# Performance work log

Measured on AMD Instinct MI355X. Metric: run time of the kernel, lower is better.

## Reference

```python
import jax, jax.numpy as jnp
import numpy as np

NEG_SLOPE = 0.2
H = 2  # num_heads (hardcoded in the torch module)


def _gat_conv(x, W, al, ar, b, src, dst, n_nodes):
    """DGL GATConv: x [N,F] -> [N,H,D]."""
    D = al.shape[1]
    h = (x @ W).reshape(n_nodes, H, D)               # [N,H,D]
    el = jnp.einsum('nhd,hd->nh', h, al)              # [N,H]
    er = jnp.einsum('nhd,hd->nh', h, ar)              # [N,H]
    e = el[src] + er[dst]                             # [E,H]
    e = jnp.where(e >= 0, e, NEG_SLOPE * e)           # LeakyReLU
    # edge softmax over incoming edges of each dst (every node has a self loop)
    m = jax.ops.segment_max(e, dst, num_segments=n_nodes)      # [N,H]
    ex = jnp.exp(e - m[dst])                                    # [E,H]
    s = jax.ops.segment_sum(ex, dst, num_segments=n_nodes)     # [N,H]
    alpha = ex / s[dst]                                         # [E,H]
    msg = alpha[:, :, None] * h[src]                             # [E,H,D]
    out = jax.ops.segment_sum(msg, dst, num_segments=n_nodes)   # [N,H,D]
    return out + b.reshape(1, H, D)


def setup_inputs() -> dict:
    key = jax.random.key(0)
    ks = jax.random.split(key, 10)
    N, E, F_IN, HID, OUT = 100000, 1600000, 128, 64, 64
    sc = 0.05
    return {
        'x':   jax.random.normal(ks[0], (N, F_IN), jnp.float32),
        'src': jax.random.randint(ks[1], (E,), 0, N, jnp.int32),
        'dst': jax.random.randint(ks[2], (E,), 0, N, jnp.int32),
        'W1':  jax.random.normal(ks[3], (F_IN, H * HID), jnp.float32) * sc,
        'al1': jax.random.normal(ks[4], (H, HID), jnp.float32) * sc,
        'ar1': jax.random.normal(ks[5], (H, HID), jnp.float32) * sc,
        'b1':  jnp.zeros((H * HID,), jnp.float32),
        'W2':  jax.random.normal(ks[6], (H * HID, H * OUT), jnp.float32) * sc,
        'al2': jax.random.normal(ks[7], (H, OUT), jnp.float32) * sc,
        'ar2': jax.random.normal(ks[8], (H, OUT), jnp.float32) * sc,
        'b2':  jnp.zeros((H * OUT,), jnp.float32),
    }


def reference(x, src, dst, W1, al1, ar1, b1, W2, al2, ar2, b2):
    N = x.shape[0]
    # dgl.add_self_loop
    loop = jnp.arange(N, dtype=src.dtype)
    s = jnp.concatenate([src, loop])
    d = jnp.concatenate([dst, loop])
    h = _gat_conv(x, W1, al1, ar1, b1, s, d, N)       # [N,H,HID]
    h = jax.nn.relu(h).reshape(N, -1)                  # flatten heads
    out = _gat_conv(h, W2, al2, ar2, b2, s, d, N)      # [N,H,OUT]
    return out.reshape(N, -1)
```

## Files before the change

### kernel.cpp

```cpp
#include <hip/hip_runtime.h>
#include <hip/hip_fp16.h>


#define NEG_SLOPE 0.2f
#define BSHIFT 8
#define ETILE 4096

typedef _Float16 half8_t __attribute__((ext_vector_type(8)));
typedef float f32x4_t __attribute__((ext_vector_type(4)));
typedef unsigned long long u64;


__global__ __launch_bounds__(256) void k_bscan(const int* __restrict__ bcnt, int nbuck,
                                               int* __restrict__ bbase,
                                               int* __restrict__ bcursor,
                                               int* __restrict__ rowStart, int N, int E) {
    __shared__ int sa[512], sb[512];
    int t = threadIdx.x;
    sa[t] = (t < nbuck) ? bcnt[t] : 0;
    sa[t + 256] = (t + 256 < nbuck) ? bcnt[t + 256] : 0;
    __syncthreads();
    int* a = sa;
    int* b = sb;
    for (int off = 1; off < 512; off <<= 1) {
        b[t] = a[t] + ((t >= off) ? a[t - off] : 0);
        int i = t + 256;
        b[i] = a[i] + ((i >= off) ? a[i - off] : 0);
        __syncthreads();
        int* tmp = a; a = b; b = tmp;
    }
    #pragma unroll
    for (int k = 0; k < 2; k++) {
        int i = t + k * 256;
        if (i <= nbuck) {
            int e_ = (i == 0) ? 0 : a[i - 1];
            bbase[i] = e_;
            if (i < nbuck) bcursor[i] = e_;
        }
    }
    if (t == 0) rowStart[N] = E;
}

__global__ __launch_bounds__(256) void k_bucket(const int* __restrict__ src,
                                                const int* __restrict__ dst, int E,
                                                int nbuck, int* __restrict__ bcursor,
                                                int* __restrict__ ebuf) {
    __shared__ int cnt[512];
    __shared__ int base[512];
    int t = threadIdx.x;
    for (int b = t; b < nbuck; b += 256) cnt[b] = 0;
    __syncthreads();
    int e0 = blockIdx.x * ETILE;
    int dv[ETILE / 256], sv[ETILE / 256];
    #pragma unroll
    for (int j = 0; j < ETILE / 256; j++) {
        int e = e0 + j * 256 + t;
        dv[j] = -1;
        if (e < E) {
            dv[j] = dst[e];
            sv[j] = src[e];
            atomicAdd(&cnt[dv[j] >> BSHIFT], 1);
        }
    }
    __syncthreads();
    for (int b = t; b < nbuck; b += 256) {
        int c = cnt[b];
        base[b] = (c > 0) ? atomicAdd(&bcursor[b], c) : 0;
    }
    __syncthreads();
    for (int b = t; b < nbuck; b += 256) cnt[b] = 0;
    __syncthreads();
    #pragma unroll
    for (int j = 0; j < ETILE / 256; j++) {
        if (dv[j] >= 0) {
            int bk = dv[j] >> BSHIFT;
            int r = atomicAdd(&cnt[bk], 1);
            ebuf[base[bk] + r] = sv[j] | ((dv[j] & ((1 << BSHIFT) - 1)) << 17);
        }
    }
}

__global__ __launch_bounds__(256) void k_build(const int* __restrict__ ebuf,
                                               const int* __restrict__ bbase,
                                               int* __restrict__ rowStart,
                                               int* __restrict__ csr, int N) {
    __shared__ int dcnt[256];
    __shared__ int sa[256], sb[256];
    __shared__ int cur[256];
    int b = blockIdx.x;
    int t = threadIdx.x;
    int lo = bbase[b], hi = bbase[b + 1];
    int n0 = b << BSHIFT;
    dcnt[t] = 0;
    __syncthreads();
    for (int p = lo + t; p < hi; p += 256)
        atomicAdd(&dcnt[((unsigned)ebuf[p]) >> 17], 1);
    __syncthreads();
    sa[t] = dcnt[t];
    __syncthreads();
    int* a = sa;
    int* bq = sb;
    for (int off = 1; off < 256; off <<= 1) {
        bq[t] = a[t] + ((t >= off) ? a[t - off] : 0);
        __syncthreads();
        int* tmp = a; a = bq; bq = tmp;
    }
    int excl = (t == 0) ? 0 : a[t - 1];
    int pos0 = lo + excl;
    if (n0 + t < N) rowStart[n0 + t] = pos0;
    cur[t] = pos0;
    __syncthreads();
    for (int p = lo + t; p < hi; p += 256) {
        int v = ebuf[p];
        int pos = atomicAdd(&cur[((unsigned)v) >> 17], 1);
        csr[pos] = v & 0x1FFFF;
    }
}


__global__ __launch_bounds__(256) void k_prep(const float* __restrict__ W1,
                                              const float* __restrict__ W2,
                                              __half* __restrict__ wh1,
                                              __half* __restrict__ wh2,
                                              int* __restrict__ bcnt, int nbuck) {
    int b = blockIdx.x;
    if (b >= 16) {
        for (int i = threadIdx.x; i < nbuck; i += 256) bcnt[i] = 0;
        return;
    }
    const float* W = (b < 8) ? W1 : W2;
    __half* Wh = (b < 8) ? wh1 : wh2;
    int q = (b & 7) * 256 + threadIdx.x;
    int r = q >> 4;
    int c = q & 15;
    int cl = c ^ (r & 7);
    float f[8];
    #pragma unroll
    for (int j = 0; j < 8; j++) f[j] = W[(size_t)(cl * 8 + j) * 128 + r];
    __half2 h0 = __floats2half2_rn(f[0], f[1]);
    __half2 h1 = __floats2half2_rn(f[2], f[3]);
    __half2 h2 = __floats2half2_rn(f[4], f[5]);
    __half2 h3 = __floats2half2_rn(f[6], f[7]);
    uint4 pk;
    pk.x = *(unsigned*)&h0;
    pk.y = *(unsigned*)&h1;
    pk.z = *(unsigned*)&h2;
    pk.w = *(unsigned*)&h3;
    *(uint4*)((char*)Wh + (size_t)q * 16) = pk;
}


__device__ __forceinline__ void g2l16(const void* g, void* l) {
    __builtin_amdgcn_global_load_lds((const __attribute__((address_space(1))) void*)g,
                                     (__attribute__((address_space(3))) void*)l, 16, 0, 0);
}

template <bool FP16IN, bool COUNT>
__global__ __launch_bounds__(256, 3) void k_gemm_fused(const void* __restrict__ Ain,
                                                       const __half* __restrict__ WhT,
                                                       __half* __restrict__ hb,
                                                       const float* __restrict__ al,
                                                       const float* __restrict__ ar,
                                                       float* __restrict__ el,
                                                       float* __restrict__ er, int M,
                                                       const int* __restrict__ dstE, int E,
                                                       int nbuck, int* __restrict__ bcnt,
                                                       int gemmBlocks) {
    __shared__ __half xs[64 * 128];
    __shared__ __half ws[128 * 128];
    int t = threadIdx.x;

    if (COUNT && (int)blockIdx.x >= gemmBlocks) {
        int* cnt = (int*)xs;
        for (int b = t; b < nbuck; b += 256) cnt[b] = 0;
        __syncthreads();
        int e0 = ((int)blockIdx.x - gemmBlocks) * ETILE;
        #pragma unroll
        for (int j = 0; j < ETILE / 256; j++) {
            int e = e0 + j * 256 + t;
            if (e < E) atomicAdd(&cnt[dstE[e] >> BSHIFT], 1);
        }
        __syncthreads();
        for (int b = t; b < nbuck; b += 256) {
            int c = cnt[b];
            if (c > 0) atomicAdd(&bcnt[b], c);
        }
        return;
    }

    int row0 = blockIdx.x * 64;
    for (int j = 0; j < 8; j++) {
        int c16 = t + j * 256;
        g2l16((const char*)WhT + (size_t)c16 * 16, (char*)ws + (size_t)c16 * 16);
    }
    if (FP16IN) {
        const char* Ah = (const char*)Ain;
        for (int j = 0; j < 4; j++) {
            int c16 = t + j * 256;
            g2l16(Ah + (size_t)row0 * 256 + (size_t)c16 * 16, (char*)xs + (size_t)c16 * 16);
        }
    } else {
        const float* A = (const float*)Ain;
        for (int j = 0; j < 8; j++) {
            int f4 = t + j * 256;
            int r = f4 >> 5;
            int gr = row0 + r;
            if (gr >= M) gr = M - 1;
            float4 v = ((const float4*)(A + (size_t)gr * 128))[f4 & 31];
            __half2 h0 = __floats2half2_rn(v.x, v.y);
            __half2 h1 = __floats2half2_rn(v.z, v.w);
            uint2 pk;
            pk.x = *(unsigned*)&h0;
            pk.y = *(unsigned*)&h1;
            int h8 = f4 & 31;
            int c = h8 >> 1, hh = h8 & 1;
            int addr8 = r * 32 + (c ^ (r & 7)) * 2 + hh;
            *(uint2*)((char*)xs + (size_t)addr8 * 8) = pk;
        }
    }
    __syncthreads();

    int wid = t >> 6, lane = t & 63;
    int l15 = lane & 15;
    int g = lane >> 4;
    int mrow = wid * 16 + l15;

    half8_t xf[4];
    #pragma unroll
    for (int ks = 0; ks < 4; ks++) {
        int c = ks * 4 + g;
        xf[ks] = *(const half8_t*)((const char*)xs + mrow * 256 + (size_t)(c ^ (mrow & 7)) * 16);
    }

    f32x4_t acc[8];
    #pragma unroll
    for (int i = 0; i < 8; i++) acc[i] = (f32x4_t){0.f, 0.f, 0.f, 0.f};

    #pragma unroll
    for (int nt = 0; nt < 8; nt++) {
        int nrow = nt * 16 + l15;
        #pragma unroll
        for (int ks = 0; ks < 4; ks++) {
            int c = ks * 4 + g;
            half8_t wf = *(const half8_t*)((const char*)ws + nrow * 256 + (size_t)(c ^ (nrow & 7)) * 16);
            acc[nt] = __builtin_amdgcn_mfma_f32_16x16x32_f16(wf, xf[ks], acc[nt], 0, 0, 0);
        }
    }

    int m = row0 + wid * 16 + l15;
    bool valid = m < M;
    float plh0 = 0.f, prh0 = 0.f, plh1 = 0.f, prh1 = 0.f;
    #pragma unroll
    for (int nt = 0; nt < 8; nt++) {
        int col0 = nt * 16 + g * 4;
        if (valid) {
            __half2 p0 = __floats2half2_rn(acc[nt][0], acc[nt][1]);
            __half2 p1 = __floats2half2_rn(acc[nt][2], acc[nt][3]);
            uint2 pk;
            pk.x = *(unsigned*)&p0;
            pk.y = *(unsigned*)&p1;
            *(uint2*)(hb + (size_t)m * 128 + col0) = pk;
        }
        float4 alv = *(const float4*)(al + col0);
        float4 arv = *(const float4*)(ar + col0);
        float pl = acc[nt][0] * alv.x + acc[nt][1] * alv.y + acc[nt][2] * alv.z + acc[nt][3] * alv.w;
        float pr = acc[nt][0] * arv.x + acc[nt][1] * arv.y + acc[nt][2] * arv.z + acc[nt][3] * arv.w;
        if (nt < 4) { plh0 += pl; prh0 += pr; }
        else       { plh1 += pl; prh1 += pr; }
    }
    plh0 += __shfl_xor(plh0, 16); plh0 += __shfl_xor(plh0, 32);
    plh1 += __shfl_xor(plh1, 16); plh1 += __shfl_xor(plh1, 32);
    prh0 += __shfl_xor(prh0, 16); prh0 += __shfl_xor(prh0, 32);
    prh1 += __shfl_xor(prh1, 16); prh1 += __shfl_xor(prh1, 32);
    if (lane < 16 && valid) {
        el[m * 2 + 0] = plh0;
        el[m * 2 + 1] = plh1;
        er[m * 2 + 0] = prh0;
        er[m * 2 + 1] = prh1;
    }
}


__device__ __forceinline__ float h2f(__half h) { return __half2float(h); }

template <bool RELU, bool FP16OUT>
__global__ __launch_bounds__(256) void k_agg(const __half* __restrict__ hb,
                                             const float* __restrict__ el,
                                             const float* __restrict__ er,
                                             const int* __restrict__ rowStart,
                                             const int* __restrict__ csr,
                                             const float* __restrict__ bias,
                                             void* __restrict__ outv, int N) {
    __shared__ u64 albuf[4][4][65];
    int wid = threadIdx.x >> 6;
    int lane = threadIdx.x & 63;
    int q = lane >> 4;
    int l = lane & 15;
    int n = (blockIdx.x * 4 + wid) * 4 + q;
    bool active = n < N;

    int rs = 0, deg = 0;
    float2 erv = make_float2(0.f, 0.f);
    if (active) {
        rs = rowStart[n];
        deg = rowStart[n + 1] - rs;
        erv = ((const float2*)er)[n];
    }

    float s0 = 0.f, s1 = 0.f;
    if (active) {
        for (int i = l; i <= deg; i += 16) {
            int s = (i == deg) ? n : csr[rs + i];
            float2 ev = ((const float2*)el)[s];
            float e0 = ev.x + erv.x;
            e0 = (e0 >= 0.f) ? e0 : NEG_SLOPE * e0;
            float e1 = ev.y + erv.y;
            e1 = (e1 >= 0.f) ? e1 : NEG_SLOPE * e1;
            float ex0 = __expf(e0);
            float ex1 = __expf(e1);
            s0 += ex0;
            s1 += ex1;
            if (i < 64) {
                __half2 eh = __floats2half2_rn(ex0, ex1);
                albuf[wid][q][i] = ((u64)(*(unsigned*)&eh) << 32) | (u64)(unsigned)s;
            }
        }
    }
    #pragma unroll
    for (int mk = 8; mk >= 1; mk >>= 1) {
        s0 += __shfl_xor(s0, mk);
        s1 += __shfl_xor(s1, mk);
    }
    bool hi = l >= 8;
    float invh = hi ? (1.0f / s1) : (1.0f / s0);

    float a0 = 0.f, a1 = 0.f, a2 = 0.f, a3 = 0.f;
    float a4 = 0.f, a5 = 0.f, a6 = 0.f, a7 = 0.f;
    if (active) {
        int cnt = deg + 1;
        int jmax = (cnt < 64) ? cnt : 64;
        #pragma unroll 4
        for (int j = 0; j < jmax; ++j) {
            u64 rec = albuf[wid][q][j];
            unsigned srcn = (unsigned)rec;
            unsigned eb = (unsigned)(rec >> 32);
            __half hx;
            *(unsigned short*)&hx = (unsigned short)(hi ? (eb >> 16) : (eb & 0xffff));
            float a = h2f(hx);
            uint4 hv = ((const uint4*)(hb + (size_t)srcn * 128))[l];
            __half2 p0 = *(__half2*)&hv.x;
            __half2 p1 = *(__half2*)&hv.y;
            __half2 p2 = *(__half2*)&hv.z;
            __half2 p3 = *(__half2*)&hv.w;
            a0 += a * h2f(p0.x);  a1 += a * h2f(p0.y);
            a2 += a * h2f(p1.x);  a3 += a * h2f(p1.y);
            a4 += a * h2f(p2.x);  a5 += a * h2f(p2.y);
            a6 += a * h2f(p3.x);  a7 += a * h2f(p3.y);
        }
        for (int j = 64; j < cnt; ++j) {
            int s = (j == deg) ? n : csr[rs + j];
            float2 ev = ((const float2*)el)[s];
            float e = hi ? (ev.y + erv.y) : (ev.x + erv.x);
            e = (e >= 0.f) ? e : NEG_SLOPE * e;
            float a = __expf(e);
            uint4 hv = ((const uint4*)(hb + (size_t)s * 128))[l];
            __half2 p0 = *(__half2*)&hv.x;
            __half2 p1 = *(__half2*)&hv.y;
            __half2 p2 = *(__half2*)&hv.z;
            __half2 p3 = *(__half2*)&hv.w;
            a0 += a * h2f(p0.x);  a1 += a * h2f(p0.y);
            a2 += a * h2f(p1.x);  a3 += a * h2f(p1.y);
            a4 += a * h2f(p2.x);  a5 += a * h2f(p2.y);
            a6 += a * h2f(p3.x);  a7 += a * h2f(p3.y);
        }

        const float4* bp = (const float4*)(bias + l * 8);
        float4 b0 = bp[0], b1 = bp[1];
        a0 = a0 * invh + b0.x;  a1 = a1 * invh + b0.y;
        a2 = a2 * invh + b0.z;  a3 = a3 * invh + b0.w;
        a4 = a4 * invh + b1.x;  a5 = a5 * invh + b1.y;
        a6 = a6 * invh + b1.z;  a7 = a7 * invh + b1.w;
        if (RELU) {
            a0 = fmaxf(a0, 0.f); a1 = fmaxf(a1, 0.f); a2 = fmaxf(a2, 0.f); a3 = fmaxf(a3, 0.f);
            a4 = fmaxf(a4, 0.f); a5 = fmaxf(a5, 0.f); a6 = fmaxf(a6, 0.f); a7 = fmaxf(a7, 0.f);
        }
        if (FP16OUT) {
            __half2 q0 = __floats2half2_rn(a0, a1);
            __half2 q1 = __floats2half2_rn(a2, a3);
            __half2 q2 = __floats2half2_rn(a4, a5);
            __half2 q3 = __floats2half2_rn(a6, a7);
            uint4 opk;
            opk.x = *(unsigned*)&q0;
            opk.y = *(unsigned*)&q1;
            opk.z = *(unsigned*)&q2;
            opk.w = *(unsigned*)&q3;
            ((uint4*)((__half*)outv + (size_t)n * 128))[l ^ (n & 7)] = opk;
        } else {
            float* op = (float*)outv + (size_t)n * 128 + l * 8;
            ((float4*)op)[0] = make_float4(a0, a1, a2, a3);
            ((float4*)op)[1] = make_float4(a4, a5, a6, a7);
        }
    }
}


static inline size_t align_up(size_t v, size_t a) { return (v + a - 1) & ~(a - 1); }

extern "C" void kernel_launch(void* const* d_in, const int* in_sizes, int n_in,
                              void* d_out, int out_size, void* d_ws, size_t ws_size,
                              hipStream_t stream) {
    const float* x   = (const float*)d_in[0];
    const int*   src = (const int*)d_in[1];
    const int*   dst = (const int*)d_in[2];
    const float* W1  = (const float*)d_in[3];
    const float* al1 = (const float*)d_in[4];
    const float* ar1 = (const float*)d_in[5];
    const float* b1  = (const float*)d_in[6];
    const float* W2  = (const float*)d_in[7];
    const float* al2 = (const float*)d_in[8];
    const float* ar2 = (const float*)d_in[9];
    const float* b2  = (const float*)d_in[10];
    float* out = (float*)d_out;

    const int N = in_sizes[0] / 128;
    const int E = in_sizes[1];
    const int NBUCK = (N + 255) >> 8;

    char* ws = (char*)d_ws;
    size_t off = 0;
    __half* bufBh = (__half*)(ws + off); off = align_up(off + (size_t)N * 128 * 2, 256);
    __half* hb    = (__half*)(ws + off); off = align_up(off + (size_t)N * 128 * 2 + 16384, 256);
    float* el   = (float*)(ws + off); off = align_up(off + (size_t)N * 2 * 4, 256);
    float* er   = (float*)(ws + off); off = align_up(off + (size_t)N * 2 * 4, 256);
    int* rowStart = (int*)(ws + off); off = align_up(off + (size_t)(N + 1) * 4, 256);
    int* csr      = (int*)(ws + off); off = align_up(off + (size_t)E * 4, 256);
    int* ebuf     = (int*)(ws + off); off = align_up(off + (size_t)E * 4, 256);
    int* bcnt     = (int*)(ws + off); off = align_up(off + (size_t)NBUCK * 4, 256);
    int* bbase    = (int*)(ws + off); off = align_up(off + (size_t)(NBUCK + 1) * 4, 256);
    int* bcursor  = (int*)(ws + off); off = align_up(off + (size_t)NBUCK * 4, 256);
    __half* wh1   = (__half*)(ws + off); off = align_up(off + (size_t)16384 * 2, 256);
    __half* wh2   = (__half*)(ws + off); off = align_up(off + (size_t)16384 * 2, 256);

    const int etile_grid = (E + ETILE - 1) / ETILE;
    const int gemm_grid = (N + 63) / 64;
    const int agg_grid = (N + 15) / 16;

    k_prep<<<17, 256, 0, stream>>>(W1, W2, wh1, wh2, bcnt, NBUCK);

    k_gemm_fused<false, true><<<gemm_grid + etile_grid, 256, 0, stream>>>(
        x, wh1, hb, al1, ar1, el, er, N, dst, E, NBUCK, bcnt, gemm_grid);

    k_bscan<<<1, 256, 0, stream>>>(bcnt, NBUCK, bbase, bcursor, rowStart, N, E);
    k_bucket<<<etile_grid, 256, 0, stream>>>(src, dst, E, NBUCK, bcursor, ebuf);
    k_build<<<NBUCK, 256, 0, stream>>>(ebuf, bbase, rowStart, csr, N);

    k_agg<true, true><<<agg_grid, 256, 0, stream>>>(hb, el, er, rowStart, csr, b1, bufBh, N);

    k_gemm_fused<true, false><<<gemm_grid, 256, 0, stream>>>(
        bufBh, wh2, hb, al2, ar2, el, er, N, nullptr, 0, 0, nullptr, gemm_grid);

    k_agg<false, false><<<agg_grid, 256, 0, stream>>>(hb, el, er, rowStart, csr, b2, out, N);
}
```

Before: 228.2 us.

## Overlap edge bucketing with layer-1 GEMM and batch aggregation gathers

Moves the dst histogram count into the weight-prep kernel and zeroes the counters with a memset. The bucket-scatter pass now runs as extra blocks at the front of the first GEMM launch, so edge bucketing overlaps the layer-1 projection instead of running as its own serialized kernel. Separately, the aggregation inner loop over cached neighbours is manually unrolled by four so that four row gathers are in flight before they are accumulated. This trades one fewer launch and better overlap for a larger fused kernel, whose bucket blocks carry extra register arrays and may be limited by the GEMM's occupancy bounds.

```diff
diff --git a/kernel.cpp b/kernel.cpp
--- a/kernel.cpp
+++ b/kernel.cpp
@@ -9,6 +9,53 @@
 typedef _Float16 half8_t __attribute__((ext_vector_type(8)));
 typedef float f32x4_t __attribute__((ext_vector_type(4)));
 typedef unsigned long long u64;
+
+
+__global__ __launch_bounds__(256) void k_prepcount(const float* __restrict__ W1,
+                                                   const float* __restrict__ W2,
+                                                   __half* __restrict__ wh1,
+                                                   __half* __restrict__ wh2,
+                                                   const int* __restrict__ dst, int E,
+                                                   int nbuck, int* __restrict__ bcnt) {
+    int b = blockIdx.x;
+    int t = threadIdx.x;
+    if (b < 16) {
+        const float* W = (b < 8) ? W1 : W2;
+        __half* Wh = (b < 8) ? wh1 : wh2;
+        int q = (b & 7) * 256 + t;
+        int r = q >> 4;
+        int c = q & 15;
+        int cl = c ^ (r & 7);
+        float f[8];
+        #pragma unroll
+        for (int j = 0; j < 8; j++) f[j] = W[(size_t)(cl * 8 + j) * 128 + r];
+        __half2 h0 = __floats2half2_rn(f[0], f[1]);
+        __half2 h1 = __floats2half2_rn(f[2], f[3]);
+        __half2 h2 = __floats2half2_rn(f[4], f[5]);
+        __half2 h3 = __floats2half2_rn(f[6], f[7]);
+        uint4 pk;
+        pk.x = *(unsigned*)&h0;
+        pk.y = *(unsigned*)&h1;
+        pk.z = *(unsigned*)&h2;
+        pk.w = *(unsigned*)&h3;
+        *(uint4*)((char*)Wh + (size_t)q * 16) = pk;
+    } else {
+        __shared__ int cnt[512];
+        for (int i = t; i < nbuck; i += 256) cnt[i] = 0;
+        __syncthreads();
+        int e0 = (b - 16) * ETILE;
+        #pragma unroll
+        for (int j = 0; j < ETILE / 256; j++) {
+            int e = e0 + j * 256 + t;
+            if (e < E) atomicAdd(&cnt[dst[e] >> BSHIFT], 1);
+        }
+        __syncthreads();
+        for (int i = t; i < nbuck; i += 256) {
+            int c = cnt[i];
+            if (c > 0) atomicAdd(&bcnt[i], c);
+        }
+    }
+}
 
 
 __global__ __launch_bounds__(256) void k_bscan(const int* __restrict__ bcnt, int nbuck,
@@ -41,44 +88,6 @@
     if (t == 0) rowStart[N] = E;
 }
 
-__global__ __launch_bounds__(256) void k_bucket(const int* __restrict__ src,
-                                                const int* __restrict__ dst, int E,
-                                                int nbuck, int* __restrict__ bcursor,
-                                                int* __restrict__ ebuf) {
-    __shared__ int cnt[512];
-    __shared__ int base[512];
-    int t = threadIdx.x;
-    for (int b = t; b < nbuck; b += 256) cnt[b] = 0;
-    __syncthreads();
-    int e0 = blockIdx.x * ETILE;
-    int dv[ETILE / 256], sv[ETILE / 256];
-    #pragma unroll
-    for (int j = 0; j < ETILE / 256; j++) {
-        int e = e0 + j * 256 + t;
-        dv[j] = -1;
-        if (e < E) {
-            dv[j] = dst[e];
-            sv[j] = src[e];
-            atomicAdd(&cnt[dv[j] >> BSHIFT], 1);
-        }
-    }
-    __syncthreads();
-    for (int b = t; b < nbuck; b += 256) {
-        int c = cnt[b];
-        base[b] = (c > 0) ? atomicAdd(&bcursor[b], c) : 0;
-    }
-    __syncthreads();
-    for (int b = t; b < nbuck; b += 256) cnt[b] = 0;
-    __syncthreads();
-    #pragma unroll
-    for (int j = 0; j < ETILE / 256; j++) {
-        if (dv[j] >= 0) {
-            int bk = dv[j] >> BSHIFT;
-            int r = atomicAdd(&cnt[bk], 1);
-            ebuf[base[bk] + r] = sv[j] | ((dv[j] & ((1 << BSHIFT) - 1)) << 17);
-        }
-    }
-}
 
 __global__ __launch_bounds__(256) void k_build(const int* __restrict__ ebuf,
                                                const int* __restrict__ bbase,
@@ -118,44 +127,12 @@
 }
 
 
-__global__ __launch_bounds__(256) void k_prep(const float* __restrict__ W1,
-                                              const float* __restrict__ W2,
-                                              __half* __restrict__ wh1,
-                                              __half* __restrict__ wh2,
-                                              int* __restrict__ bcnt, int nbuck) {
-    int b = blockIdx.x;
-    if (b >= 16) {
-        for (int i = threadIdx.x; i < nbuck; i += 256) bcnt[i] = 0;
-        return;
-    }
-    const float* W = (b < 8) ? W1 : W2;
-    __half* Wh = (b < 8) ? wh1 : wh2;
-    int q = (b & 7) * 256 + threadIdx.x;
-    int r = q >> 4;
-    int c = q & 15;
-    int cl = c ^ (r & 7);
-    float f[8];
-    #pragma unroll
-    for (int j = 0; j < 8; j++) f[j] = W[(size_t)(cl * 8 + j) * 128 + r];
-    __half2 h0 = __floats2half2_rn(f[0], f[1]);
-    __half2 h1 = __floats2half2_rn(f[2], f[3]);
-    __half2 h2 = __floats2half2_rn(f[4], f[5]);
-    __half2 h3 = __floats2half2_rn(f[6], f[7]);
-    uint4 pk;
-    pk.x = *(unsigned*)&h0;
-    pk.y = *(unsigned*)&h1;
-    pk.z = *(unsigned*)&h2;
-    pk.w = *(unsigned*)&h3;
-    *(uint4*)((char*)Wh + (size_t)q * 16) = pk;
-}
-
-
 __device__ __forceinline__ void g2l16(const void* g, void* l) {
     __builtin_amdgcn_global_load_lds((const __attribute__((address_space(1))) void*)g,
                                      (__attribute__((address_space(3))) void*)l, 16, 0, 0);
 }
 
-template <bool FP16IN, bool COUNT>
+template <bool FP16IN, bool BUCKET>
 __global__ __launch_bounds__(256, 3) void k_gemm_fused(const void* __restrict__ Ain,
                                                        const __half* __restrict__ WhT,
                                                        __half* __restrict__ hb,
@@ -163,32 +140,52 @@
                                                        const float* __restrict__ ar,
                                                        float* __restrict__ el,
                                                        float* __restrict__ er, int M,
+                                                       const int* __restrict__ srcE,
                                                        const int* __restrict__ dstE, int E,
-                                                       int nbuck, int* __restrict__ bcnt,
-                                                       int gemmBlocks) {
+                                                       int nbuck, int* __restrict__ bcursor,
+                                                       int* __restrict__ ebuf,
+                                                       int bucketBlocks) {
     __shared__ __half xs[64 * 128];
     __shared__ __half ws[128 * 128];
     int t = threadIdx.x;
 
-    if (COUNT && (int)blockIdx.x >= gemmBlocks) {
+    if (BUCKET && (int)blockIdx.x < bucketBlocks) {
         int* cnt = (int*)xs;
+        int* base = cnt + 512;
         for (int b = t; b < nbuck; b += 256) cnt[b] = 0;
         __syncthreads();
-        int e0 = ((int)blockIdx.x - gemmBlocks) * ETILE;
+        int e0 = (int)blockIdx.x * ETILE;
+        int dv[ETILE / 256], sv[ETILE / 256];
         #pragma unroll
         for (int j = 0; j < ETILE / 256; j++) {
             int e = e0 + j * 256 + t;
-            if (e < E) atomicAdd(&cnt[dstE[e] >> BSHIFT], 1);
+            dv[j] = -1;
+            if (e < E) {
+                dv[j] = dstE[e];
+                sv[j] = srcE[e];
+                atomicAdd(&cnt[dv[j] >> BSHIFT], 1);
+            }
         }
         __syncthreads();
         for (int b = t; b < nbuck; b += 256) {
             int c = cnt[b];
-            if (c > 0) atomicAdd(&bcnt[b], c);
+            base[b] = (c > 0) ? atomicAdd(&bcursor[b], c) : 0;
+        }
+        __syncthreads();
+        for (int b = t; b < nbuck; b += 256) cnt[b] = 0;
+        __syncthreads();
+        #pragma unroll
+        for (int j = 0; j < ETILE / 256; j++) {
+            if (dv[j] >= 0) {
+                int bk = dv[j] >> BSHIFT;
+                int r = atomicAdd(&cnt[bk], 1);
+                ebuf[base[bk] + r] = sv[j] | ((dv[j] & ((1 << BSHIFT) - 1)) << 17);
+            }
         }
         return;
     }
 
-    int row0 = blockIdx.x * 64;
+    int row0 = (BUCKET ? ((int)blockIdx.x - bucketBlocks) : (int)blockIdx.x) * 64;
     for (int j = 0; j < 8; j++) {
         int c16 = t + j * 256;
         g2l16((const char*)WhT + (size_t)c16 * 16, (char*)ws + (size_t)c16 * 16);
@@ -339,15 +336,41 @@
     if (active) {
         int cnt = deg + 1;
         int jmax = (cnt < 64) ? cnt : 64;
-        #pragma unroll 4
-        for (int j = 0; j < jmax; ++j) {
+        int j = 0;
+        for (; j + 4 <= jmax; j += 4) {
+            u64 r0 = albuf[wid][q][j + 0];
+            u64 r1 = albuf[wid][q][j + 1];
+            u64 r2 = albuf[wid][q][j + 2];
+            u64 r3 = albuf[wid][q][j + 3];
+            uint4 v0 = ((const uint4*)(hb + (size_t)(unsigned)r0 * 128))[l];
+            uint4 v1 = ((const uint4*)(hb + (size_t)(unsigned)r1 * 128))[l];
+            uint4 v2 = ((const uint4*)(hb + (size_t)(unsigned)r2 * 128))[l];
+            uint4 v3 = ((const uint4*)(hb + (size_t)(unsigned)r3 * 128))[l];
+            #pragma unroll
+            for (int kk = 0; kk < 4; kk++) {
+                u64 rec = (kk == 0) ? r0 : (kk == 1) ? r1 : (kk == 2) ? r2 : r3;
+                uint4 hv = (kk == 0) ? v0 : (kk == 1) ? v1 : (kk == 2) ? v2 : v3;
+                unsigned eb = (unsigned)(rec >> 32);
+                __half hx;
+                *(unsigned short*)&hx = (unsigned short)(hi ? (eb >> 16) : (eb & 0xffff));
+                float a = h2f(hx);
+                __half2 p0 = *(__half2*)&hv.x;
+                __half2 p1 = *(__half2*)&hv.y;
+                __half2 p2 = *(__half2*)&hv.z;
+                __half2 p3 = *(__half2*)&hv.w;
+                a0 += a * h2f(p0.x);  a1 += a * h2f(p0.y);
+                a2 += a * h2f(p1.x);  a3 += a * h2f(p1.y);
+                a4 += a * h2f(p2.x);  a5 += a * h2f(p2.y);
+                a6 += a * h2f(p3.x);  a7 += a * h2f(p3.y);
+            }
+        }
+        for (; j < jmax; ++j) {
             u64 rec = albuf[wid][q][j];
-            unsigned srcn = (unsigned)rec;
             unsigned eb = (unsigned)(rec >> 32);
             __half hx;
             *(unsigned short*)&hx = (unsigned short)(hi ? (eb >> 16) : (eb & 0xffff));
             float a = h2f(hx);
-            uint4 hv = ((const uint4*)(hb + (size_t)srcn * 128))[l];
+            uint4 hv = ((const uint4*)(hb + (size_t)(unsigned)rec * 128))[l];
             __half2 p0 = *(__half2*)&hv.x;
             __half2 p1 = *(__half2*)&hv.y;
             __half2 p2 = *(__half2*)&hv.z;
@@ -357,8 +380,8 @@
             a4 += a * h2f(p2.x);  a5 += a * h2f(p2.y);
             a6 += a * h2f(p3.x);  a7 += a * h2f(p3.y);
         }
-        for (int j = 64; j < cnt; ++j) {
-            int s = (j == deg) ? n : csr[rs + j];
+        for (int jj = 64; jj < cnt; ++jj) {
+            int s = (jj == deg) ? n : csr[rs + jj];
             float2 ev = ((const float2*)el)[s];
             float e = hi ? (ev.y + erv.y) : (ev.x + erv.x);
             e = (e >= 0.f) ? e : NEG_SLOPE * e;
@@ -445,19 +468,19 @@
     const int gemm_grid = (N + 63) / 64;
     const int agg_grid = (N + 15) / 16;
 
-    k_prep<<<17, 256, 0, stream>>>(W1, W2, wh1, wh2, bcnt, NBUCK);
-
-    k_gemm_fused<false, true><<<gemm_grid + etile_grid, 256, 0, stream>>>(
-        x, wh1, hb, al1, ar1, el, er, N, dst, E, NBUCK, bcnt, gemm_grid);
-
+    hipMemsetAsync(bcnt, 0, (size_t)NBUCK * 4, stream);
+    k_prepcount<<<16 + etile_grid, 256, 0, stream>>>(W1, W2, wh1, wh2, dst, E, NBUCK, bcnt);
     k_bscan<<<1, 256, 0, stream>>>(bcnt, NBUCK, bbase, bcursor, rowStart, N, E);
-    k_bucket<<<etile_grid, 256, 0, stream>>>(src, dst, E, NBUCK, bcursor, ebuf);
+
+    k_gemm_fused<false, true><<<etile_grid + gemm_grid, 256, 0, stream>>>(
+        x, wh1, hb, al1, ar1, el, er, N, src, dst, E, NBUCK, bcursor, ebuf, etile_grid);
+
     k_build<<<NBUCK, 256, 0, stream>>>(ebuf, bbase, rowStart, csr, N);
 
     k_agg<true, true><<<agg_grid, 256, 0, stream>>>(hb, el, er, rowStart, csr, b1, bufBh, N);
 
     k_gemm_fused<true, false><<<gemm_grid, 256, 0, stream>>>(
-        bufBh, wh2, hb, al2, ar2, el, er, N, nullptr, 0, 0, nullptr, gemm_grid);
+        bufBh, wh2, hb, al2, ar2, el, er, N, nullptr, nullptr, 0, 0, nullptr, nullptr, 0);
 
     k_agg<false, false><<<agg_grid, 256, 0, stream>>>(hb, el, er, rowStart, csr, b2, out, N);
 }
```

After: 225.8 us. Within noise of the previous version (-1.0%).
